# Optimization experiments

Hardware: AMD Instinct MI355X
Metric: run time of the kernel (lower is better)

## Reference

```python
import jax, jax.numpy as jnp
import numpy as np

K = 6
D_IN = 128
D_OUT = 128
N_COARSE = 4000
N_FINE = 40000


def setup_inputs() -> dict:
    key = jax.random.key(0)
    k1, k2, k3, k4, k5 = jax.random.split(key, 5)
    x_coarse = jax.random.normal(k1, (N_COARSE, D_IN), dtype=jnp.float32)
    pos_coarse = jax.random.uniform(k2, (N_COARSE, 3), dtype=jnp.float32)
    pos_fine = jax.random.uniform(k3, (N_FINE, 3), dtype=jnp.float32)
    # nnx.Linear params: lecun_normal kernel, zero bias (use small random for generality)
    W = jax.random.normal(k4, (D_IN, D_OUT), dtype=jnp.float32) / np.sqrt(D_IN)
    b = jax.random.normal(k5, (D_OUT,), dtype=jnp.float32) * 0.01
    return {"x_coarse": x_coarse, "pos_coarse": pos_coarse, "pos_fine": pos_fine, "W": W, "b": b}


def reference(x_coarse, pos_coarse, pos_fine, W, b):
    # dense pairwise L2 distances [Nf, Nc] (faithful to the original's full matrix)
    distances = jnp.linalg.norm(pos_fine[:, None, :] - pos_coarse[None, :, :], axis=-1)
    # full argsort then slice, matching the original (incl. tie-break order)
    knn_idx = jnp.argsort(distances, axis=1)[:, :K]        # [Nf, K]
    gathered = x_coarse[knn_idx]                            # [Nf, K, d_in]
    interp = jnp.mean(gathered, axis=1)                     # [Nf, d_in]
    return interp @ W + b                                   # [Nf, d_out]
```

## Files before the change

### kernel.cpp

```cpp
#include <hip/hip_runtime.h>
#include <cstdint>

#define NCOARSE 4000
#define NFINE   40000
#define DIM     128
#define GRES    8
#define CELLH   0.125f
#define CAP_C   40
#define CAP_F   160
#define CHUNKS  5
#define SCAP    768
#define NS      172
#define NYG     500

__device__ __forceinline__ uint64_t min64(uint64_t a, uint64_t b) { return a < b ? a : b; }
__device__ __forceinline__ uint64_t max64(uint64_t a, uint64_t b) { return a > b ? a : b; }
__device__ __forceinline__ int cell_coord(float x) {
    int c = (int)(x * 8.0f);
    return c < 0 ? 0 : (c > 7 ? 7 : c);
}

__global__ __launch_bounds__(256) void k_zero(int* __restrict__ p) {
    p[blockIdx.x * 256 + threadIdx.x] = 0;
}

__global__ __launch_bounds__(256) void k_build(const float* __restrict__ pc,
                                               const float* __restrict__ pf,
                                               const float* __restrict__ xc,
                                               const float* __restrict__ W,
                                               int* __restrict__ cntC, int* __restrict__ cntF,
                                               float4* __restrict__ ptsC, float4* __restrict__ srtF,
                                               float* __restrict__ Y) {
    __shared__ float xs[8][DIM];
    const int bid = blockIdx.x, tid = threadIdx.x;
    if (bid < NS) {
        const int i = bid * 256 + tid;
        if (i < NCOARSE) {
            const float x = pc[3*i], y = pc[3*i+1], z = pc[3*i+2];
            const int c = (cell_coord(z) << 6) | (cell_coord(y) << 3) | cell_coord(x);
            const int slot = atomicAdd(&cntC[c], 1);
            if (slot < CAP_C) ptsC[c * CAP_C + slot] = make_float4(x, y, z, __int_as_float(i));
        } else if (i < NCOARSE + NFINE) {
            const int j = i - NCOARSE;
            const float x = pf[3*j], y = pf[3*j+1], z = pf[3*j+2];
            const int c = (cell_coord(z) << 6) | (cell_coord(y) << 3) | cell_coord(x);
            const int slot = atomicAdd(&cntF[c], 1);
            if (slot < CAP_F) srtF[c * CAP_F + slot] = make_float4(x, y, z, __int_as_float(j));
        }
    } else {
        const int g  = bid - NS;
        const int r0 = g * 8;
        reinterpret_cast<float4*>(xs)[tid] =
            reinterpret_cast<const float4*>(xc + r0 * DIM)[tid];
        __syncthreads();
        const int rq = tid >> 5;
        const int jq = tid & 31;
        float a0 = 0.f, a1 = 0.f, a2 = 0.f, a3 = 0.f;
        #pragma unroll 4
        for (int k = 0; k < DIM; ++k) {
            const float a = xs[rq][k];
            const float4 wv = *reinterpret_cast<const float4*>(W + k * DIM + jq * 4);
            a0 += a * wv.x; a1 += a * wv.y; a2 += a * wv.z; a3 += a * wv.w;
        }
        *reinterpret_cast<float4*>(Y + (r0 + rq) * DIM + jq * 4) = make_float4(a0, a1, a2, a3);
    }
}

__device__ __forceinline__ void merge_with(uint64_t w[7], int mask) {
    uint64_t v[16];
    #pragma unroll
    for (int r = 0; r < 7; ++r) v[r] = w[r];
    v[7] = ~0ull; v[8] = ~0ull;
    #pragma unroll
    for (int r = 0; r < 7; ++r)
        v[9 + r] = __shfl_xor((unsigned long long)w[6 - r], mask);
    #pragma unroll
    for (int k = 8; k >= 1; k >>= 1) {
        #pragma unroll
        for (int i = 0; i < 16; ++i) {
            if ((i & k) == 0) {
                const uint64_t lo = min64(v[i], v[i | k]);
                v[i | k] = max64(v[i], v[i | k]);
                v[i] = lo;
            }
        }
    }
    #pragma unroll
    for (int r = 0; r < 7; ++r) w[r] = v[r];
}

__device__ __forceinline__ bool done_check(uint64_t k7, float fx, float fy, float fz,
                                           int ix, int iy, int iz, int s) {
    const float d7 = __uint_as_float((uint32_t)(k7 >> 32));
    float clear = 1e30f;
    if (ix - s >= 0) clear = fminf(clear, __fsub_rn(fx, (float)(ix - s) * CELLH));
    if (ix + s <= 6) clear = fminf(clear, __fsub_rn((float)(ix + s + 1) * CELLH, fx));
    if (iy - s >= 0) clear = fminf(clear, __fsub_rn(fy, (float)(iy - s) * CELLH));
    if (iy + s <= 6) clear = fminf(clear, __fsub_rn((float)(iy + s + 1) * CELLH, fy));
    if (iz - s >= 0) clear = fminf(clear, __fsub_rn(fz, (float)(iz - s) * CELLH));
    if (iz + s <= 6) clear = fminf(clear, __fsub_rn((float)(iz + s + 1) * CELLH, fz));
    return d7 < clear * clear * 0.9999f;
}

#define INS(p) { \
    const float ddx = __fsub_rn(fx, (p).x); \
    const float ddy = __fsub_rn(fy, (p).y); \
    const float ddz = __fsub_rn(fz, (p).z); \
    const float d2  = __fadd_rn(__fadd_rn(__fmul_rn(ddx, ddx), __fmul_rn(ddy, ddy)), \
                                __fmul_rn(ddz, ddz)); \
    const uint64_t v = ((uint64_t)__float_as_uint(d2) << 32) | (uint32_t)__float_as_uint((p).w); \
    if (v < own[6]) { \
        own[6] = min64(own[6], max64(own[5], v)); \
        own[5] = min64(own[5], max64(own[4], v)); \
        own[4] = min64(own[4], max64(own[3], v)); \
        own[3] = min64(own[3], max64(own[2], v)); \
        own[2] = min64(own[2], max64(own[1], v)); \
        own[1] = min64(own[1], max64(own[0], v)); \
        own[0] = min64(own[0], v); \
    } }

__global__ __launch_bounds__(256) void k_main(
    const float*  __restrict__ Y,
    const float*  __restrict__ bias,
    const int*    __restrict__ cntC,
    const int*    __restrict__ cntF,
    const float4* __restrict__ ptsG,
    const float4* __restrict__ srtF,
    float* __restrict__ out)
{
    __shared__ float4 spts[SCAP];
    __shared__ int rBeg[32], rLds[32];
    __shared__ int idx6[32][6];
    __shared__ int forig[32];
    __shared__ int metaT[1];

    const int bid  = blockIdx.x;
    const int tid  = threadIdx.x;
    const int cell = bid & 511;
    const int chunk= bid >> 9;

    const int ctot = min(cntF[cell], CAP_F);
    const int base = chunk * 32;
    const int npts = min(32, ctot - base);
    if (npts <= 0) return;

    const int fl  = tid >> 3;
    const int par = tid & 7;
    const int ix = cell & 7, iy = (cell >> 3) & 7, iz = cell >> 6;

    const int srcf = min(fl, npts - 1);
    const float4 fp = srtF[cell * CAP_F + base + srcf];
    const float fx = fp.x, fy = fp.y, fz = fp.z;
    if (par == 0) forig[fl] = (fl < npts) ? __float_as_int(fp.w) : -1;

    const int bx0 = max(ix - 1, 0), bx1 = min(ix + 1, 7);
    const int by0 = max(iy - 1, 0), by1 = min(iy + 1, 7);
    const int bz0 = max(iz - 1, 0), bz1 = min(iz + 1, 7);
    const int nx = bx1 - bx0 + 1, ny = by1 - by0 + 1, nz = bz1 - bz0 + 1;
    const int ncell = nx * ny * nz;

    if (tid < 32) {
        const bool valid = tid < ncell;
        int len = 0, bg = 0;
        if (valid) {
            const int ex = bx0 + tid % nx;
            const int rem = tid / nx;
            const int ey = by0 + rem % ny;
            const int ez = bz0 + rem / ny;
            const int cc = (ez << 6) | (ey << 3) | ex;
            len = min(cntC[cc], CAP_C);
            bg  = cc * CAP_C;
        }
        int x = len;
        #pragma unroll
        for (int o = 1; o < 32; o <<= 1) {
            const int v = __shfl_up(x, o);
            if (tid >= o) x += v;
        }
        rBeg[tid] = valid ? bg : 0;
        rLds[tid] = valid ? (x - len) : 0x7fffffff;
        if (tid == ncell - 1) metaT[0] = x;
    }
    __syncthreads();

    const int total  = metaT[0];
    const bool staged = (total <= SCAP);
    if (staged) {
        for (int g = tid; g < total; g += 256) {
            int lo = 0, hi = 31;
            while (lo < hi) { const int mid = (lo + hi + 1) >> 1; if (rLds[mid] <= g) lo = mid; else hi = mid - 1; }
            spts[g] = ptsG[rBeg[lo] + (g - rLds[lo])];
        }
    }
    __syncthreads();

    uint64_t own[7];
    #pragma unroll
    for (int r = 0; r < 7; ++r) own[r] = ~0ull;

    if (staged) {
        #pragma unroll 4
        for (int i = par; i < total; i += 8) { float4 p = spts[i]; INS(p) }
    } else {
        for (int cz = bz0; cz <= bz1; ++cz)
            for (int cy = by0; cy <= by1; ++cy)
                for (int cx = bx0; cx <= bx1; ++cx) {
                    const int cc = (cz << 6) | (cy << 3) | cx;
                    const int len = min(cntC[cc], CAP_C);
                    const int bg  = cc * CAP_C;
                    for (int i = par; i < len; i += 8) { float4 p = ptsG[bg + i]; INS(p) }
                }
    }

    uint64_t mg[7];
    #pragma unroll
    for (int r = 0; r < 7; ++r) mg[r] = own[r];
    merge_with(mg, 1); merge_with(mg, 2); merge_with(mg, 4);
    bool done = done_check(mg[6], fx, fy, fz, ix, iy, iz, 1);

    for (int s = 2; s <= 7; ++s) {
        if (__all(done)) break;
        if (!done) {
            for (int dz = -s; dz <= s; ++dz) {
                const int cz = iz + dz;
                if ((unsigned)cz >= (unsigned)GRES) continue;
                const bool fz_face = (dz == -s) | (dz == s);
                for (int dy = -s; dy <= s; ++dy) {
                    const int cy = iy + dy;
                    if ((unsigned)cy >= (unsigned)GRES) continue;
                    const bool yz_face = fz_face | (dy == -s) | (dy == s);
                    for (int dx = -s; dx <= s; ++dx) {
                        if (!yz_face && dx > -s && dx < s) continue;
                        const int cx = ix + dx;
                        if ((unsigned)cx >= (unsigned)GRES) continue;
                        if (cx >= bx0 && cx <= bx1 && cy >= by0 && cy <= by1 &&
                            cz >= bz0 && cz <= bz1) continue;
                        const int cc = (cz << 6) | (cy << 3) | cx;
                        const int len = min(cntC[cc], CAP_C);
                        const int bg  = cc * CAP_C;
                        for (int i = par; i < len; i += 8) { float4 p = ptsG[bg + i]; INS(p) }
                    }
                }
            }
            #pragma unroll
            for (int r = 0; r < 7; ++r) mg[r] = own[r];
            merge_with(mg, 1); merge_with(mg, 2); merge_with(mg, 4);
            done = done_check(mg[6], fx, fy, fz, ix, iy, iz, s);
        }
    }

    if (par == 0) {
        int i5 = (int)(uint32_t)mg[5];
        const int i6 = (int)(uint32_t)mg[6];
        const float d5 = sqrtf(__uint_as_float((uint32_t)(mg[5] >> 32)));
        const float d6 = sqrtf(__uint_as_float((uint32_t)(mg[6] >> 32)));
        if (d5 == d6 && i6 < i5) i5 = i6;
        idx6[fl][0] = (int)(uint32_t)mg[0];
        idx6[fl][1] = (int)(uint32_t)mg[1];
        idx6[fl][2] = (int)(uint32_t)mg[2];
        idx6[fl][3] = (int)(uint32_t)mg[3];
        idx6[fl][4] = (int)(uint32_t)mg[4];
        idx6[fl][5] = i5;
    }
    __syncthreads();

    {
        const int fr = forig[fl];
        if (fr >= 0) {
            const int id0 = idx6[fl][0], id1 = idx6[fl][1], id2 = idx6[fl][2];
            const int id3 = idx6[fl][3], id4 = idx6[fl][4], id5 = idx6[fl][5];
            constexpr float inv6 = 1.0f / 6.0f;
            #pragma unroll
            for (int k = 0; k < 4; ++k) {
                const int q = (k * 8 + par) * 4;
                const float4 y0 = *reinterpret_cast<const float4*>(Y + id0 * DIM + q);
                const float4 y1 = *reinterpret_cast<const float4*>(Y + id1 * DIM + q);
                const float4 y2 = *reinterpret_cast<const float4*>(Y + id2 * DIM + q);
                const float4 y3 = *reinterpret_cast<const float4*>(Y + id3 * DIM + q);
                const float4 y4 = *reinterpret_cast<const float4*>(Y + id4 * DIM + q);
                const float4 y5 = *reinterpret_cast<const float4*>(Y + id5 * DIM + q);
                const float4 bv = *reinterpret_cast<const float4*>(bias + q);
                float4 o;
                o.x = (y0.x + y1.x + y2.x + y3.x + y4.x + y5.x) * inv6 + bv.x;
                o.y = (y0.y + y1.y + y2.y + y3.y + y4.y + y5.y) * inv6 + bv.y;
                o.z = (y0.z + y1.z + y2.z + y3.z + y4.z + y5.z) * inv6 + bv.z;
                o.w = (y0.w + y1.w + y2.w + y3.w + y4.w + y5.w) * inv6 + bv.w;
                *reinterpret_cast<float4*>(out + fr * DIM + q) = o;
            }
        }
    }
}

extern "C" void kernel_launch(void* const* d_in, const int* in_sizes, int n_in,
                              void* d_out, int out_size, void* d_ws, size_t ws_size,
                              hipStream_t stream) {
    const float* xc = (const float*)d_in[0];
    const float* pc = (const float*)d_in[1];
    const float* pf = (const float*)d_in[2];
    const float* W  = (const float*)d_in[3];
    const float* b  = (const float*)d_in[4];
    float* out = (float*)d_out;

    int*    cntC = (int*)d_ws;
    int*    cntF = (int*)((char*)d_ws + 2048);
    float4* ptsC = (float4*)((char*)d_ws + 4096);
    float4* srtF = (float4*)((char*)d_ws + 331776);
    float*  Y    = (float*)((char*)d_ws + 1642496);

    k_zero <<<dim3(4),          dim3(256), 0, stream>>>((int*)d_ws);
    k_build<<<dim3(NS + NYG),   dim3(256), 0, stream>>>(pc, pf, xc, W, cntC, cntF, ptsC, srtF, Y);
    k_main <<<dim3(512 * CHUNKS), dim3(256), 0, stream>>>(Y, b, cntC, cntF, ptsC, srtF, out);
}
```

Before: 57.85 us.

## Shrink kNN blocks to 16 points, register-tile Y GEMM, pop-min merge

New measurement: 59.78 us. 3.3% more time.

```diff
diff --git a/kernel.cpp b/kernel.cpp
--- a/kernel.cpp
+++ b/kernel.cpp
@@ -8,10 +8,11 @@
 #define CELLH   0.125f
 #define CAP_C   40
 #define CAP_F   160
-#define CHUNKS  5
-#define SCAP    768
+#define PPB     16
+#define CHUNKS  10
+#define SCAP    640
 #define NS      172
-#define NYG     500
+#define NYG     125
 
 __device__ __forceinline__ uint64_t min64(uint64_t a, uint64_t b) { return a < b ? a : b; }
 __device__ __forceinline__ uint64_t max64(uint64_t a, uint64_t b) { return a > b ? a : b; }
@@ -31,7 +32,7 @@
                                                int* __restrict__ cntC, int* __restrict__ cntF,
                                                float4* __restrict__ ptsC, float4* __restrict__ srtF,
                                                float* __restrict__ Y) {
-    __shared__ float xs[8][DIM];
+    __shared__ float xs[32][DIM];
     const int bid = blockIdx.x, tid = threadIdx.x;
     if (bid < NS) {
         const int i = bid * 256 + tid;
@@ -49,44 +50,55 @@
         }
     } else {
         const int g  = bid - NS;
-        const int r0 = g * 8;
-        reinterpret_cast<float4*>(xs)[tid] =
-            reinterpret_cast<const float4*>(xc + r0 * DIM)[tid];
+        const int r0 = g * 32;
+        #pragma unroll
+        for (int t = 0; t < 4; ++t)
+            reinterpret_cast<float4*>(xs)[tid + t * 256] =
+                reinterpret_cast<const float4*>(xc + r0 * DIM)[tid + t * 256];
         __syncthreads();
         const int rq = tid >> 5;
         const int jq = tid & 31;
-        float a0 = 0.f, a1 = 0.f, a2 = 0.f, a3 = 0.f;
-        #pragma unroll 4
+        float acc[4][4];
+        #pragma unroll
+        for (int i = 0; i < 4; ++i)
+            #pragma unroll
+            for (int j = 0; j < 4; ++j) acc[i][j] = 0.f;
+        #pragma unroll 2
         for (int k = 0; k < DIM; ++k) {
-            const float a = xs[rq][k];
             const float4 wv = *reinterpret_cast<const float4*>(W + k * DIM + jq * 4);
-            a0 += a * wv.x; a1 += a * wv.y; a2 += a * wv.z; a3 += a * wv.w;
-        }
-        *reinterpret_cast<float4*>(Y + (r0 + rq) * DIM + jq * 4) = make_float4(a0, a1, a2, a3);
-    }
-}
-
-__device__ __forceinline__ void merge_with(uint64_t w[7], int mask) {
-    uint64_t v[16];
+            #pragma unroll
+            for (int i = 0; i < 4; ++i) {
+                const float a = xs[rq + 8 * i][k];
+                acc[i][0] += a * wv.x; acc[i][1] += a * wv.y;
+                acc[i][2] += a * wv.z; acc[i][3] += a * wv.w;
+            }
+        }
+        #pragma unroll
+        for (int i = 0; i < 4; ++i)
+            *reinterpret_cast<float4*>(Y + (r0 + rq + 8 * i) * DIM + jq * 4) =
+                make_float4(acc[i][0], acc[i][1], acc[i][2], acc[i][3]);
+    }
+}
+
+__device__ __forceinline__ void popmin_merge(const uint64_t own[7], uint64_t mg[7]) {
+    uint64_t a0 = own[0], a1 = own[1], a2 = own[2], a3 = own[3],
+             a4 = own[4], a5 = own[5], a6 = own[6];
     #pragma unroll
-    for (int r = 0; r < 7; ++r) v[r] = w[r];
-    v[7] = ~0ull; v[8] = ~0ull;
-    #pragma unroll
-    for (int r = 0; r < 7; ++r)
-        v[9 + r] = __shfl_xor((unsigned long long)w[6 - r], mask);
-    #pragma unroll
-    for (int k = 8; k >= 1; k >>= 1) {
-        #pragma unroll
-        for (int i = 0; i < 16; ++i) {
-            if ((i & k) == 0) {
-                const uint64_t lo = min64(v[i], v[i | k]);
-                v[i | k] = max64(v[i], v[i | k]);
-                v[i] = lo;
-            }
-        }
-    }
-    #pragma unroll
-    for (int r = 0; r < 7; ++r) w[r] = v[r];
+    for (int r = 0; r < 7; ++r) {
+        uint64_t m = a0;
+        m = min64(m, __shfl_xor((unsigned long long)m, 1));
+        m = min64(m, __shfl_xor((unsigned long long)m, 2));
+        m = min64(m, __shfl_xor((unsigned long long)m, 4));
+        mg[r] = m;
+        const bool win = (a0 == m);
+        a0 = win ? a1 : a0;
+        a1 = win ? a2 : a1;
+        a2 = win ? a3 : a2;
+        a3 = win ? a4 : a3;
+        a4 = win ? a5 : a4;
+        a5 = win ? a6 : a5;
+        a6 = win ? ~0ull : a6;
+    }
 }
 
 __device__ __forceinline__ bool done_check(uint64_t k7, float fx, float fy, float fz,
@@ -119,7 +131,7 @@
         own[0] = min64(own[0], v); \
     } }
 
-__global__ __launch_bounds__(256) void k_main(
+__global__ __launch_bounds__(128) void k_main(
     const float*  __restrict__ Y,
     const float*  __restrict__ bias,
     const int*    __restrict__ cntC,
@@ -130,8 +142,8 @@
 {
     __shared__ float4 spts[SCAP];
     __shared__ int rBeg[32], rLds[32];
-    __shared__ int idx6[32][6];
-    __shared__ int forig[32];
+    __shared__ int idx6[PPB][6];
+    __shared__ int forig[PPB];
     __shared__ int metaT[1];
 
     const int bid  = blockIdx.x;
@@ -140,8 +152,8 @@
     const int chunk= bid >> 9;
 
     const int ctot = min(cntF[cell], CAP_F);
-    const int base = chunk * 32;
-    const int npts = min(32, ctot - base);
+    const int base = chunk * PPB;
+    const int npts = min(PPB, ctot - base);
     if (npts <= 0) return;
 
     const int fl  = tid >> 3;
@@ -186,7 +198,7 @@
     const int total  = metaT[0];
     const bool staged = (total <= SCAP);
     if (staged) {
-        for (int g = tid; g < total; g += 256) {
+        for (int g = tid; g < total; g += 128) {
             int lo = 0, hi = 31;
             while (lo < hi) { const int mid = (lo + hi + 1) >> 1; if (rLds[mid] <= g) lo = mid; else hi = mid - 1; }
             spts[g] = ptsG[rBeg[lo] + (g - rLds[lo])];
@@ -213,9 +225,7 @@
     }
 
     uint64_t mg[7];
-    #pragma unroll
-    for (int r = 0; r < 7; ++r) mg[r] = own[r];
-    merge_with(mg, 1); merge_with(mg, 2); merge_with(mg, 4);
+    popmin_merge(own, mg);
     bool done = done_check(mg[6], fx, fy, fz, ix, iy, iz, 1);
 
     for (int s = 2; s <= 7; ++s) {
@@ -242,9 +252,7 @@
                     }
                 }
             }
-            #pragma unroll
-            for (int r = 0; r < 7; ++r) mg[r] = own[r];
-            merge_with(mg, 1); merge_with(mg, 2); merge_with(mg, 4);
+            popmin_merge(own, mg);
             done = done_check(mg[6], fx, fy, fz, ix, iy, iz, s);
         }
     }
@@ -307,7 +315,7 @@
     float4* srtF = (float4*)((char*)d_ws + 331776);
     float*  Y    = (float*)((char*)d_ws + 1642496);
 
-    k_zero <<<dim3(4),          dim3(256), 0, stream>>>((int*)d_ws);
-    k_build<<<dim3(NS + NYG),   dim3(256), 0, stream>>>(pc, pf, xc, W, cntC, cntF, ptsC, srtF, Y);
-    k_main <<<dim3(512 * CHUNKS), dim3(256), 0, stream>>>(Y, b, cntC, cntF, ptsC, srtF, out);
-}
+    k_zero <<<dim3(4),            dim3(256), 0, stream>>>((int*)d_ws);
+    k_build<<<dim3(NS + NYG),     dim3(256), 0, stream>>>(pc, pf, xc, W, cntC, cntF, ptsC, srtF, Y);
+    k_main <<<dim3(512 * CHUNKS), dim3(128), 0, stream>>>(Y, b, cntC, cntF, ptsC, srtF, out);
+}
```
